# Performance work log

Hardware: AMD Instinct MI355X
Metric: run time of the kernel (lower is better)

The kernel has to match this reference:

```python
import jax, jax.numpy as jnp
import numpy as np

B, T, C, H = 2, 2048, 1024, 16
HD = C // H  # 64
EPS = 1e-5


def _ln(x, g, b):
    mu = jnp.mean(x, axis=-1, keepdims=True)
    var = jnp.var(x, axis=-1, keepdims=True)
    return (x - mu) * jax.lax.rsqrt(var + EPS) * g + b


def setup_inputs() -> dict:
    key = jax.random.key(0)
    ks = jax.random.split(key, 8)
    s = lambda n: 1.0 / np.sqrt(n)
    return {
        "x": jax.random.normal(ks[0], (B, T, C), dtype=jnp.float32),
        "ln1_g": jnp.ones((C,), jnp.float32), "ln1_b": jnp.zeros((C,), jnp.float32),
        "ln2_g": jnp.ones((C,), jnp.float32), "ln2_b": jnp.zeros((C,), jnp.float32),
        "w_in": jax.random.normal(ks[1], (C, 3 * C), jnp.float32) * s(C),
        "b_in": jnp.zeros((3 * C,), jnp.float32),
        "w_out": jax.random.normal(ks[2], (C, C), jnp.float32) * s(C),
        "b_out": jnp.zeros((C,), jnp.float32),
        "w_fc": jax.random.normal(ks[3], (C, 4 * C), jnp.float32) * s(C),
        "b_fc": jnp.zeros((4 * C,), jnp.float32),
        "w_proj": jax.random.normal(ks[4], (4 * C, C), jnp.float32) * s(4 * C),
        "b_proj": jnp.zeros((C,), jnp.float32),
    }


def reference(x, ln1_g, ln1_b, ln2_g, ln2_b, w_in, b_in, w_out, b_out,
              w_fc, b_fc, w_proj, b_proj):
    # --- residual 1: x + attn(ln1(x)) ---
    h = _ln(x, ln1_g, ln1_b)
    qkv = h @ w_in + b_in                          # (B,T,3C)
    # reshape to (B,T,H,3*HD) then chunk per head (matches torch code exactly)
    qkv = qkv.reshape(B, T, H, 3 * HD).transpose(0, 2, 1, 3)  # (B,H,T,3*HD)
    q, k, v = jnp.split(qkv, 3, axis=-1)           # each (B,H,T,HD)
    att = jnp.einsum('bhqd,bhkd->bhqk', q, k) / np.sqrt(HD)
    causal = jnp.tril(jnp.ones((T, T), bool))
    att = jnp.where(causal, att, -jnp.inf)
    att = jax.nn.softmax(att, axis=-1)
    o = jnp.einsum('bhqk,bhkd->bhqd', att, v)      # (B,H,T,HD)
    o = o.transpose(0, 2, 1, 3).reshape(B, T, C)
    x1 = x + (o @ w_out + b_out)
    # --- ln2 applied to residual stream, then residual 2 on top of ln2 output ---
    y = _ln(x1, ln2_g, ln2_b)
    mlp = jax.nn.gelu(y @ w_fc + b_fc, approximate=False) @ w_proj + b_proj
    return y + mlp
```

## Files before the change

### kernel.cpp

```cpp
#include <hip/hip_runtime.h>
#include <hip/hip_bf16.h>
#include <math.h>

typedef __bf16 bf16;
typedef __bf16 bf16x8 __attribute__((ext_vector_type(8)));
typedef __bf16 bf16x4 __attribute__((ext_vector_type(4)));
typedef float floatx4 __attribute__((ext_vector_type(4)));

#define B_ 2
#define T_ 2048
#define C_ 1024
#define H_ 16
#define HD_ 64


__device__ __forceinline__ void gload_lds16(const bf16* g, bf16* l) {
    __builtin_amdgcn_global_load_lds(
        (const __attribute__((address_space(1))) unsigned int*)(g),
        (__attribute__((address_space(3))) unsigned int*)(l), 16, 0, 0);
}

__global__ __launch_bounds__(256) void transpose_all(
        const float* __restrict__ w_in, const float* __restrict__ w_out,
        const float* __restrict__ w_fc, const float* __restrict__ w_proj,
        bf16* __restrict__ o_in, bf16* __restrict__ o_out,
        bf16* __restrict__ o_fc, bf16* __restrict__ o_proj) {
    __shared__ float shf[64 * 33];
    int t = blockIdx.x;
    int tid = threadIdx.x;
    if (t < 7168) {
        const float* src; bf16* dst; int K, N, idx;
        if (t < 3072) { src = w_in; dst = o_in; K = 1024; N = 3072; idx = t; }
        else          { src = w_fc; dst = o_fc; K = 1024; N = 4096; idx = t - 3072; }
        int ntx = N >> 5;
        int nt = (idx % ntx) * 32, kt = (idx / ntx) * 32;
        int tx = tid & 31, ty = tid >> 5;
        #pragma unroll
        for (int i = 0; i < 32; i += 8)
            shf[(ty + i) * 33 + tx] = src[(size_t)(kt + ty + i) * N + nt + tx];
        __syncthreads();
        #pragma unroll
        for (int i = 0; i < 32; i += 8)
            dst[(size_t)(nt + ty + i) * K + kt + tx] = (bf16)shf[tx * 33 + ty + i];
    } else {
        const float* src; bf16* dst; int K, idx;
        if (t < 7680) { src = w_out;  dst = o_out;  K = 1024; idx = t - 7168; }
        else          { src = w_proj; dst = o_proj; K = 4096; idx = t - 7680; }
        const int N = 1024;
        int n0 = (idx & 31) * 32, k0 = (idx >> 5) * 64;
        int col = tid & 31, kr = tid >> 5;
        #pragma unroll
        for (int s = 0; s < 8; s++)
            shf[(kr + s * 8) * 33 + col] = src[(size_t)(k0 + kr + s * 8) * N + n0 + col];
        __syncthreads();
        int tl = tid >> 6, l = tid & 63;
        int ntl = tl & 1, kcl = tl >> 1;
        int rr = ntl * 16 + (l & 15);
        int qd = l >> 4;
        bf16x8 v;
        #pragma unroll
        for (int e = 0; e < 8; e++)
            v[e] = (bf16)shf[(kcl * 32 + qd * 8 + e) * 33 + rr];
        size_t nt_g = (n0 >> 4) + ntl, kc_g = (k0 >> 5) + kcl;
        *(bf16x8*)(dst + (nt_g * (K >> 5) + kc_g) * 512 + l * 8) = v;
    }
}

__global__ __launch_bounds__(256) void ln_kernel(const float* __restrict__ x,
                                                 const float* __restrict__ g,
                                                 const float* __restrict__ b,
                                                 bf16* __restrict__ out_b,
                                                 float* __restrict__ out_f) {
    int row = blockIdx.x;
    int tid = threadIdx.x;
    const float* xr = x + (size_t)row * C_;
    float4 v = ((const float4*)xr)[tid];
    float s  = v.x + v.y + v.z + v.w;
    float ss = v.x * v.x + v.y * v.y + v.z * v.z + v.w * v.w;
    #pragma unroll
    for (int off = 32; off; off >>= 1) {
        s  += __shfl_down(s, off);
        ss += __shfl_down(ss, off);
    }
    __shared__ float red[8];
    int wid = tid >> 6;
    if ((tid & 63) == 0) { red[wid] = s; red[wid + 4] = ss; }
    __syncthreads();
    s  = red[0] + red[1] + red[2] + red[3];
    ss = red[4] + red[5] + red[6] + red[7];
    float mean = s * (1.0f / C_);
    float var  = ss * (1.0f / C_) - mean * mean;
    float rstd = rsqrtf(var + 1e-5f);
    float4 gv = ((const float4*)g)[tid];
    float4 bv = ((const float4*)b)[tid];
    float o0 = (v.x - mean) * rstd * gv.x + bv.x;
    float o1 = (v.y - mean) * rstd * gv.y + bv.y;
    float o2 = (v.z - mean) * rstd * gv.z + bv.z;
    float o3 = (v.w - mean) * rstd * gv.w + bv.w;
    bf16x4 ob = { (bf16)o0, (bf16)o1, (bf16)o2, (bf16)o3 };
    ((bf16x4*)out_b)[(size_t)row * 256 + tid] = ob;
    if (out_f) {
        float4 of; of.x = o0; of.y = o1; of.z = o2; of.w = o3;
        ((float4*)out_f)[(size_t)row * 256 + tid] = of;
    }
}

__device__ __forceinline__ float gelu_fast(float x) {
    float z2 = 1.5957691216f * (x + 0.044715f * x * x * x);
    float e = __expf(z2);
    float t = 1.0f - 2.0f * __builtin_amdgcn_rcpf(e + 1.0f);
    return 0.5f * x * (1.0f + t);
}

template<int MODE>
__global__ __launch_bounds__(256) void gemm128(const bf16* __restrict__ A,
                                               const bf16* __restrict__ Bt,
                                               const float* __restrict__ bias,
                                               void* __restrict__ out,
                                               int M, int N, int K) {
    __shared__ __align__(16) bf16 smem[2 * 128 * 64];
    bf16* As = smem;
    bf16* Bs = smem + 128 * 64;

    int m0 = blockIdx.y * 128, n0 = blockIdx.x * 128;
    int tid = threadIdx.x;
    int wid = __builtin_amdgcn_readfirstlane(tid >> 6);
    int lane = tid & 63;
    int lm = lane & 15, quad = lane >> 4;
    int wm = (wid & 1) * 64;
    int wn = (wid >> 1) * 64;
    int lrow = lane >> 3;
    int lcol = (((lane & 7) ^ lrow)) * 8;

    const bf16* Ablk = A  + (size_t)m0 * K;
    const bf16* Bblk = Bt + (size_t)n0 * K;

    floatx4 acc[4][4];
    #pragma unroll
    for (int i = 0; i < 4; i++)
        #pragma unroll
        for (int j = 0; j < 4; j++) { floatx4 z = {0.f, 0.f, 0.f, 0.f}; acc[i][j] = z; }

    for (int k0 = 0; k0 < K; k0 += 64) {
        __syncthreads();
        #pragma unroll
        for (int c = 0; c < 4; c++) {
            int row = wid * 32 + c * 8;
            gload_lds16(Ablk + (size_t)(row + lrow) * K + k0 + lcol, As + row * 64);
        }
        #pragma unroll
        for (int c = 0; c < 4; c++) {
            int row = wid * 32 + c * 8;
            gload_lds16(Bblk + (size_t)(row + lrow) * K + k0 + lcol, Bs + row * 64);
        }
        __syncthreads();
        #pragma unroll
        for (int kc = 0; kc < 2; kc++) {
            bf16x8 af[4], bfr[4];
            #pragma unroll
            for (int i = 0; i < 4; i++)
                af[i] = *(const bf16x8*)(As + (wm + i * 16 + lm) * 64 +
                                         ((((kc << 2) + quad) ^ (lm & 7)) << 3));
            #pragma unroll
            for (int j = 0; j < 4; j++)
                bfr[j] = *(const bf16x8*)(Bs + (wn + j * 16 + lm) * 64 +
                                          ((((kc << 2) + quad) ^ (lm & 7)) << 3));
            #pragma unroll
            for (int i = 0; i < 4; i++)
                #pragma unroll
                for (int j = 0; j < 4; j++)
                    acc[i][j] = __builtin_amdgcn_mfma_f32_16x16x32_bf16(af[i], bfr[j], acc[i][j], 0, 0, 0);
        }
    }

    if (MODE == 0) {
        #pragma unroll
        for (int i = 0; i < 4; i++)
            #pragma unroll
            for (int j = 0; j < 4; j++) {
                int mbase = m0 + wm + i * 16 + quad * 4;
                int n     = n0 + wn + j * 16 + lm;
                float bsn = bias[n];
                #pragma unroll
                for (int r = 0; r < 4; r++)
                    ((bf16*)out)[(size_t)(mbase + r) * N + n] = (bf16)(acc[i][j][r] + bsn);
            }
    } else {
        bf16* ob = (bf16*)out;
        #pragma unroll
        for (int nh = 0; nh < 2; nh++) {
            __syncthreads();
            if ((wn >> 6) == nh) {
                #pragma unroll
                for (int i = 0; i < 4; i++)
                    #pragma unroll
                    for (int j = 0; j < 4; j++) {
                        int n = n0 + wn + j * 16 + lm;
                        float bsn = bias[n];
                        #pragma unroll
                        for (int r = 0; r < 4; r++)
                            smem[(wm + i * 16 + quad * 4 + r) * 68 + j * 16 + lm] =
                                (bf16)gelu_fast(acc[i][j][r] + bsn);
                    }
            }
            __syncthreads();
            #pragma unroll
            for (int p = 0; p < 4; p++) {
                int tl = wid * 4 + p;
                int mtl = tl >> 1, kclp = tl & 1;
                bf16x8 v = *(const bf16x8*)&smem[(mtl * 16 + lm) * 68 + kclp * 32 + quad * 8];
                int kcl = nh * 2 + kclp;
                *(bf16x8*)(ob + (((size_t)((m0 >> 4) + mtl) * (N >> 5) + (n0 >> 5) + kcl) * 512)
                           + lane * 8) = v;
            }
        }
    }
}

__global__ __launch_bounds__(256) void gemm_direct(const bf16* __restrict__ Af,
                                                   const bf16* __restrict__ Bf,
                                                   const float* __restrict__ bias,
                                                   const float* __restrict__ add,
                                                   float* __restrict__ out,
                                                   int M, int N, int K) {
    int lin = blockIdx.x;
    int xcd = lin & 7, loc = lin >> 3;
    int m0 = ((xcd << 2) | (loc & 3)) * 128;
    int n0 = (loc >> 2) * 64;
    int tid = threadIdx.x;
    int wid = __builtin_amdgcn_readfirstlane(tid >> 6);
    int lane = tid & 63;
    int lm = lane & 15, quad = lane >> 4;
    int wm = (wid & 1) * 64, wn = (wid >> 1) * 32;
    int KC = K >> 5;
    const bf16* Ab = Af + ((size_t)((m0 + wm) >> 4) * KC) * 512 + lane * 8;
    const bf16* Bb = Bf + ((size_t)((n0 + wn) >> 4) * KC) * 512 + lane * 8;

    floatx4 acc[4][2];
    #pragma unroll
    for (int i = 0; i < 4; i++)
        #pragma unroll
        for (int j = 0; j < 2; j++) { floatx4 z = {0.f, 0.f, 0.f, 0.f}; acc[i][j] = z; }

    bf16x8 ac[4][2], bc[2][2], an[4][2], bn[2][2];
    #pragma unroll
    for (int i = 0; i < 4; i++)
        #pragma unroll
        for (int c = 0; c < 2; c++)
            ac[i][c] = *(const bf16x8*)(Ab + ((size_t)i * KC + c) * 512);
    #pragma unroll
    for (int j = 0; j < 2; j++)
        #pragma unroll
        for (int c = 0; c < 2; c++)
            bc[j][c] = *(const bf16x8*)(Bb + ((size_t)j * KC + c) * 512);

    for (int kc0 = 0; kc0 < KC; kc0 += 2) {
        bool pre = (kc0 + 2) < KC;
        if (pre) {
            #pragma unroll
            for (int i = 0; i < 4; i++)
                #pragma unroll
                for (int c = 0; c < 2; c++)
                    an[i][c] = *(const bf16x8*)(Ab + ((size_t)i * KC + kc0 + 2 + c) * 512);
            #pragma unroll
            for (int j = 0; j < 2; j++)
                #pragma unroll
                for (int c = 0; c < 2; c++)
                    bn[j][c] = *(const bf16x8*)(Bb + ((size_t)j * KC + kc0 + 2 + c) * 512);
        }
        #pragma unroll
        for (int c = 0; c < 2; c++)
            #pragma unroll
            for (int i = 0; i < 4; i++)
                #pragma unroll
                for (int j = 0; j < 2; j++)
                    acc[i][j] = __builtin_amdgcn_mfma_f32_16x16x32_bf16(ac[i][c], bc[j][c], acc[i][j], 0, 0, 0);
        if (pre) {
            #pragma unroll
            for (int i = 0; i < 4; i++)
                #pragma unroll
                for (int c = 0; c < 2; c++) ac[i][c] = an[i][c];
            #pragma unroll
            for (int j = 0; j < 2; j++)
                #pragma unroll
                for (int c = 0; c < 2; c++) bc[j][c] = bn[j][c];
        }
    }

    #pragma unroll
    for (int i = 0; i < 4; i++)
        #pragma unroll
        for (int j = 0; j < 2; j++) {
            int mbase = m0 + wm + i * 16 + quad * 4;
            int n     = n0 + wn + j * 16 + lm;
            float bsn = bias[n];
            #pragma unroll
            for (int r = 0; r < 4; r++) {
                size_t idx = (size_t)(mbase + r) * N + n;
                out[idx] = acc[i][j][r] + bsn + add[idx];
            }
        }
}

#define QT_ 128
#define KT_ 64

__global__ __launch_bounds__(512) void attn_mfma_kernel(const bf16* __restrict__ qkv,
                                                        bf16* __restrict__ of) {
    int bh = blockIdx.x;
    int b = bh >> 4, h = bh & 15;
    int q0 = (gridDim.y - 1 - blockIdx.y) * QT_;
    int tid = threadIdx.x, wid = tid >> 6, lane = tid & 63;
    int lm = lane & 15, quad = lane >> 4;
    int sw = lm & 7;
    int r0 = q0 + wid * 16;

    const bf16* base = qkv + (size_t)b * T_ * (3 * C_) + h * (3 * HD_);

    __shared__ __align__(16) bf16 Ks[KT_][72];
    __shared__ __align__(16) bf16 Vt[HD_][72];
    __shared__ __align__(16) bf16 PsT[8][16][64];

    bf16x8 qf[2];
    #pragma unroll
    for (int kc = 0; kc < 2; kc++) {
        bf16x8 t = *(const bf16x8*)(base + (size_t)(r0 + lm) * (3 * C_) + kc * 32 + quad * 8);
        #pragma unroll
        for (int e = 0; e < 8; e++) t[e] = (bf16)((float)t[e] * 0.125f);
        qf[kc] = t;
    }

    floatx4 acc_o[4];
    #pragma unroll
    for (int dn = 0; dn < 4; dn++) { floatx4 z = {0.f, 0.f, 0.f, 0.f}; acc_o[dn] = z; }
    float mst = -1e30f, lst = 0.0f;

    int srow = tid >> 3;
    int scol = (tid & 7) * 8;

    int kmax = q0 + QT_;
    for (int k0 = 0; k0 < kmax; k0 += KT_) {
        bf16x8 kv = *(const bf16x8*)(base + (size_t)(k0 + srow) * (3 * C_) + HD_ + scol);
        bf16x8 vv = *(const bf16x8*)(base + (size_t)(k0 + srow) * (3 * C_) + 2 * HD_ + scol);
        __syncthreads();
        *(bf16x8*)(&Ks[srow][scol]) = kv;
        {
            int c = scol >> 3;
            int pk = ((srow >> 3) ^ c) * 8 + (srow & 7);
            #pragma unroll
            for (int j = 0; j < 8; j++) Vt[scol + j][pk] = vv[j];
        }
        __syncthreads();

        if (k0 <= r0 + 15) {
            floatx4 st[4];
            #pragma unroll
            for (int bn = 0; bn < 4; bn++) { floatx4 z = {0.f, 0.f, 0.f, 0.f}; st[bn] = z; }
            #pragma unroll
            for (int kc = 0; kc < 2; kc++) {
                bf16x8 kf[4];
                #pragma unroll
                for (int bn = 0; bn < 4; bn++)
                    kf[bn] = *(const bf16x8*)(&Ks[bn * 16 + lm][kc * 32 + quad * 8]);
                #pragma unroll
                for (int bn = 0; bn < 4; bn++)
                    st[bn] = __builtin_amdgcn_mfma_f32_16x16x32_bf16(kf[bn], qf[kc], st[bn], 0, 0, 0);
            }

            float vv_[4][4];
            float rm = -1e30f;
            if (k0 + KT_ - 1 > r0) {
                int gq = r0 + lm;
                #pragma unroll
                for (int bn = 0; bn < 4; bn++)
                    #pragma unroll
                    for (int r = 0; r < 4; r++) {
                        int key = k0 + bn * 16 + quad * 4 + r;
                        float sv = (key <= gq) ? st[bn][r] : -1e30f;
                        vv_[bn][r] = sv;
                        rm = fmaxf(rm, sv);
                    }
            } else {
                #pragma unroll
                for (int bn = 0; bn < 4; bn++)
                    #pragma unroll
                    for (int r = 0; r < 4; r++) {
                        vv_[bn][r] = st[bn][r];
                        rm = fmaxf(rm, st[bn][r]);
                    }
            }
            rm = fmaxf(rm, __shfl_xor(rm, 16));
            rm = fmaxf(rm, __shfl_xor(rm, 32));
            float mnew = fmaxf(mst, rm);
            float alpha = __expf(mst - mnew);
            mst = mnew;
            float ps = 0.f;
            #pragma unroll
            for (int bn = 0; bn < 4; bn++) {
                float p0 = __expf(vv_[bn][0] - mnew);
                float p1 = __expf(vv_[bn][1] - mnew);
                float p2 = __expf(vv_[bn][2] - mnew);
                float p3 = __expf(vv_[bn][3] - mnew);
                ps += (p0 + p1) + (p2 + p3);
                bf16x4 pk = { (bf16)p0, (bf16)p1, (bf16)p2, (bf16)p3 };
                int kb = bn * 2 + (quad >> 1);
                int col = ((kb ^ sw) << 3) + (quad & 1) * 4;
                *(bf16x4*)(&PsT[wid][lm][col]) = pk;
            }
            ps += __shfl_xor(ps, 16);
            ps += __shfl_xor(ps, 32);
            lst = lst * alpha + ps;

            #pragma unroll
            for (int r = 0; r < 4; r++) {
                float ar = __shfl(alpha, quad * 4 + r);
                #pragma unroll
                for (int dn = 0; dn < 4; dn++) acc_o[dn][r] *= ar;
            }

            __asm__ volatile("s_waitcnt lgkmcnt(0)" ::: "memory");

            #pragma unroll
            for (int kc = 0; kc < 2; kc++) {
                bf16x8 pa = *(const bf16x8*)(&PsT[wid][lm][((kc * 4 + quad) ^ sw) << 3]);
                bf16x8 vfr[4];
                #pragma unroll
                for (int dn = 0; dn < 4; dn++) {
                    int d = dn * 16 + lm;
                    int swd = (d >> 3) & 7;
                    vfr[dn] = *(const bf16x8*)(&Vt[d][(((kc * 4 + quad) ^ swd) << 3)]);
                }
                #pragma unroll
                for (int dn = 0; dn < 4; dn++)
                    acc_o[dn] = __builtin_amdgcn_mfma_f32_16x16x32_bf16(pa, vfr[dn], acc_o[dn], 0, 0, 0);
            }
        }
    }

    float il = 1.0f / lst;
    #pragma unroll
    for (int r = 0; r < 4; r++) {
        float ir = __shfl(il, quad * 4 + r);
        #pragma unroll
        for (int dn = 0; dn < 4; dn++)
            PsT[wid][quad * 4 + r][dn * 16 + lm] = (bf16)(acc_o[dn][r] * ir);
    }
    __asm__ volatile("s_waitcnt lgkmcnt(0)" ::: "memory");
    size_t mtb = ((size_t)b * T_ + r0) >> 4;
    #pragma unroll
    for (int kcl = 0; kcl < 2; kcl++) {
        bf16x8 v = *(const bf16x8*)&PsT[wid][lm][kcl * 32 + quad * 8];
        *(bf16x8*)(of + (mtb * (C_ >> 5) + (h * 2 + kcl)) * 512 + lane * 8) = v;
    }
}

extern "C" void kernel_launch(void* const* d_in, const int* in_sizes, int n_in,
                              void* d_out, int out_size, void* d_ws, size_t ws_size,
                              hipStream_t stream) {
    (void)in_sizes; (void)n_in; (void)out_size; (void)ws_size;
    const float* x      = (const float*)d_in[0];
    const float* ln1_g  = (const float*)d_in[1];
    const float* ln1_b  = (const float*)d_in[2];
    const float* ln2_g  = (const float*)d_in[3];
    const float* ln2_b  = (const float*)d_in[4];
    const float* w_in   = (const float*)d_in[5];
    const float* b_in   = (const float*)d_in[6];
    const float* w_out  = (const float*)d_in[7];
    const float* b_out  = (const float*)d_in[8];
    const float* w_fc   = (const float*)d_in[9];
    const float* b_fc   = (const float*)d_in[10];
    const float* w_proj = (const float*)d_in[11];
    const float* b_proj = (const float*)d_in[12];

    char* ws = (char*)d_ws;
    const size_t MB = 1024 * 1024;
    bf16*  w_inT   = (bf16*)(ws + 0);
    bf16*  w_outF  = (bf16*)(ws + 6 * MB);
    bf16*  w_fcT   = (bf16*)(ws + 8 * MB);
    bf16*  w_projF = (bf16*)(ws + 16 * MB);
    bf16*  qkv     = (bf16*)(ws + 24 * MB);
    bf16*  fc_frag = (bf16*)(ws + 24 * MB);
    bf16*  o_frag  = (bf16*)(ws + 56 * MB);
    bf16*  y_b     = (bf16*)(ws + 56 * MB);
    bf16*  h_b     = (bf16*)(ws + 64 * MB);
    float* x1      = (float*)(ws + 64 * MB);
    float* y_f     = (float*)(ws + 80 * MB);

    const int M = B_ * T_;

    transpose_all<<<9728, 256, 0, stream>>>(w_in, w_out, w_fc, w_proj,
                                            w_inT, w_outF, w_fcT, w_projF);

    ln_kernel<<<M, 256, 0, stream>>>(x, ln1_g, ln1_b, h_b, nullptr);
    gemm128<0><<<dim3(3 * C_ / 128, M / 128), 256, 0, stream>>>(h_b, w_inT, b_in,
                                                                qkv, M, 3 * C_, C_);
    attn_mfma_kernel<<<dim3(B_ * H_, T_ / QT_), 512, 0, stream>>>(qkv, o_frag);
    gemm_direct<<<512, 256, 0, stream>>>(o_frag, w_outF, b_out, x, x1, M, C_, C_);
    ln_kernel<<<M, 256, 0, stream>>>(x1, ln2_g, ln2_b, y_b, y_f);
    gemm128<1><<<dim3(4 * C_ / 128, M / 128), 256, 0, stream>>>(y_b, w_fcT, b_fc,
                                                                fc_frag, M, 4 * C_, C_);
    gemm_direct<<<512, 256, 0, stream>>>(fc_frag, w_projF, b_proj, y_f,
                                         (float*)d_out, M, C_, 4 * C_);
}
```

Before: 350.9 us.

## Replace 128-tile GEMM with double-buffered 256x256 pipelined GEMM and triple-buffer direct GEMM

The QKV and FC GEMMs move from a 128x128, single-buffered LDS kernel to a 256x256-tile, 512-thread kernel. It double-buffers A/B in LDS, interleaves async global-to-LDS loads with quarter-tile MFMA groups, uses explicit barriers and vmcnt waits, raises wave priority around the MFMAs, and remaps blocks across XCDs. The direct-fragment GEMM gets a three-stage register prefetch ring in place of two stages. The aim is to hide memory latency and raise MFMA utilisation. The cost is much higher register and LDS use (128 KB smem) and fewer, larger blocks, which could hurt occupancy or tail balance.

```diff
diff --git a/kernel.cpp b/kernel.cpp
--- a/kernel.cpp
+++ b/kernel.cpp
@@ -112,117 +112,186 @@
     return 0.5f * x * (1.0f + t);
 }
 
+#define BAR() do { __builtin_amdgcn_sched_barrier(0); __builtin_amdgcn_s_barrier(); __builtin_amdgcn_sched_barrier(0); } while (0)
+#define VMC6() asm volatile("s_waitcnt vmcnt(6)" ::: "memory")
+#define VMC0() asm volatile("s_waitcnt vmcnt(0)" ::: "memory")
+
+#define LOAD_A(AS, QM) \
+  { _Pragma("unroll") for (int i_ = 0; i_ < 4; i_++) { \
+      const int r_ = wm128 + ((QM) * 4 + i_) * 16 + lm; \
+      _Pragma("unroll") for (int kc_ = 0; kc_ < 2; kc_++) \
+        aR[i_][kc_] = *(const bf16x8*)((AS) + r_ * 64 + ((((kc_ << 2) | quad) ^ (lm & 7)) << 3)); } }
+
+#define LOAD_B(BS, QN) \
+  { _Pragma("unroll") for (int j_ = 0; j_ < 2; j_++) { \
+      const int r_ = wn64 + ((QN) * 2 + j_) * 16 + lm; \
+      _Pragma("unroll") for (int kc_ = 0; kc_ < 2; kc_++) \
+        bR[QN][j_][kc_] = *(const bf16x8*)((BS) + r_ * 64 + ((((kc_ << 2) | quad) ^ (lm & 7)) << 3)); } }
+
+#define MFMA_Q(QM, QN) \
+  { __builtin_amdgcn_s_setprio(1); \
+    _Pragma("unroll") for (int i_ = 0; i_ < 4; i_++) \
+    _Pragma("unroll") for (int j_ = 0; j_ < 2; j_++) \
+    _Pragma("unroll") for (int kc_ = 0; kc_ < 2; kc_++) \
+      acc[(QM) * 4 + i_][(QN) * 2 + j_] = __builtin_amdgcn_mfma_f32_16x16x32_bf16( \
+          aR[i_][kc_], bR[QN][j_][kc_], acc[(QM) * 4 + i_][(QN) * 2 + j_], 0, 0, 0); \
+    __builtin_amdgcn_s_setprio(0); }
+
+#define STG(gb, lb, r0v, k0v) \
+    gload_lds16((gb) + (size_t)((r0v) + sr8) * K + (k0v) + scb, (lb) + ((r0v) + wid * 8) * 64)
+
 template<int MODE>
-__global__ __launch_bounds__(256) void gemm128(const bf16* __restrict__ A,
-                                               const bf16* __restrict__ Bt,
-                                               const float* __restrict__ bias,
-                                               void* __restrict__ out,
-                                               int M, int N, int K) {
-    __shared__ __align__(16) bf16 smem[2 * 128 * 64];
-    bf16* As = smem;
-    bf16* Bs = smem + 128 * 64;
-
-    int m0 = blockIdx.y * 128, n0 = blockIdx.x * 128;
+__global__ __launch_bounds__(512, 2) void gemm256(const bf16* __restrict__ A,
+                                                  const bf16* __restrict__ Bt,
+                                                  const float* __restrict__ bias,
+                                                  void* __restrict__ out,
+                                                  int M, int N, int K) {
+    (void)M;
+    __shared__ __align__(16) bf16 smem[4 * 256 * 64];
+    bf16* As0 = smem;
+    bf16* Bs0 = smem + 1 * 256 * 64;
+    bf16* As1 = smem + 2 * 256 * 64;
+    bf16* Bs1 = smem + 3 * 256 * 64;
+
+    int ntn = N >> 8;
+    int lin = blockIdx.x;
+    int id  = (lin & 7) * (gridDim.x >> 3) + (lin >> 3);
+    int mt = id / ntn, nt = id - mt * ntn;
+    int m0 = mt << 8, n0 = nt << 8;
+
     int tid = threadIdx.x;
     int wid = __builtin_amdgcn_readfirstlane(tid >> 6);
     int lane = tid & 63;
     int lm = lane & 15, quad = lane >> 4;
-    int wm = (wid & 1) * 64;
-    int wn = (wid >> 1) * 64;
-    int lrow = lane >> 3;
-    int lcol = (((lane & 7) ^ lrow)) * 8;
+    int wm128 = (wid & 1) * 128;
+    int wn64  = (wid >> 1) * 64;
 
     const bf16* Ablk = A  + (size_t)m0 * K;
     const bf16* Bblk = Bt + (size_t)n0 * K;
 
-    floatx4 acc[4][4];
-    #pragma unroll
-    for (int i = 0; i < 4; i++)
-        #pragma unroll
-        for (int j = 0; j < 4; j++) { floatx4 z = {0.f, 0.f, 0.f, 0.f}; acc[i][j] = z; }
-
-    for (int k0 = 0; k0 < K; k0 += 64) {
-        __syncthreads();
-        #pragma unroll
-        for (int c = 0; c < 4; c++) {
-            int row = wid * 32 + c * 8;
-            gload_lds16(Ablk + (size_t)(row + lrow) * K + k0 + lcol, As + row * 64);
-        }
-        #pragma unroll
-        for (int c = 0; c < 4; c++) {
-            int row = wid * 32 + c * 8;
-            gload_lds16(Bblk + (size_t)(row + lrow) * K + k0 + lcol, Bs + row * 64);
-        }
-        __syncthreads();
-        #pragma unroll
-        for (int kc = 0; kc < 2; kc++) {
-            bf16x8 af[4], bfr[4];
-            #pragma unroll
-            for (int i = 0; i < 4; i++)
-                af[i] = *(const bf16x8*)(As + (wm + i * 16 + lm) * 64 +
-                                         ((((kc << 2) + quad) ^ (lm & 7)) << 3));
-            #pragma unroll
-            for (int j = 0; j < 4; j++)
-                bfr[j] = *(const bf16x8*)(Bs + (wn + j * 16 + lm) * 64 +
-                                          ((((kc << 2) + quad) ^ (lm & 7)) << 3));
-            #pragma unroll
-            for (int i = 0; i < 4; i++)
-                #pragma unroll
-                for (int j = 0; j < 4; j++)
-                    acc[i][j] = __builtin_amdgcn_mfma_f32_16x16x32_bf16(af[i], bfr[j], acc[i][j], 0, 0, 0);
-        }
+    int sr8 = wid * 8 + (lane >> 3);
+    int scb = ((lane & 7) ^ (lane >> 3)) << 3;
+
+    floatx4 acc[8][4];
+    #pragma unroll
+    for (int f = 0; f < 8; f++)
+        #pragma unroll
+        for (int g = 0; g < 4; g++) { floatx4 z = {0.f, 0.f, 0.f, 0.f}; acc[f][g] = z; }
+    bf16x8 aR[4][2], bR[2][2][2];
+
+    int nI = K >> 7;
+
+    STG(Ablk, As0, 0, 0);   STG(Ablk, As0, 64, 0);
+    STG(Ablk, As0, 128, 0); STG(Ablk, As0, 192, 0);
+    STG(Bblk, Bs0, 0, 0);   STG(Bblk, Bs0, 64, 0);
+    STG(Bblk, Bs0, 128, 0); STG(Bblk, Bs0, 192, 0);
+    STG(Ablk, As1, 0, 64);  STG(Ablk, As1, 128, 64);
+    STG(Bblk, Bs1, 0, 64);  STG(Bblk, Bs1, 64, 64);
+    STG(Ablk, As1, 64, 64); STG(Ablk, As1, 192, 64);
+    VMC6();
+    BAR();
+
+    for (int it = 0; it < nI; it++) {
+        int kE = (2 * it + 2) << 6;
+        int kO = (2 * it + 3) << 6;
+        int kT = (2 * it + 1) << 6;
+        bool nl = (it + 1 < nI);
+        LOAD_A(As0, 0); LOAD_B(Bs0, 0);
+        STG(Bblk, Bs1, 128, kT); STG(Bblk, Bs1, 192, kT);
+        BAR(); MFMA_Q(0, 0); BAR();
+        LOAD_B(Bs0, 1);
+        if (nl) { STG(Ablk, As0, 0, kE); STG(Ablk, As0, 128, kE); }
+        BAR(); MFMA_Q(0, 1); BAR();
+        LOAD_A(As0, 1);
+        if (nl) { STG(Bblk, Bs0, 0, kE); STG(Bblk, Bs0, 64, kE); }
+        BAR(); MFMA_Q(1, 0); BAR();
+        if (nl) { STG(Ablk, As0, 64, kE); STG(Ablk, As0, 192, kE); }
+        BAR(); MFMA_Q(1, 1);
+        if (nl) { VMC6(); } else { VMC0(); }
+        BAR();
+        LOAD_A(As1, 0); LOAD_B(Bs1, 0);
+        if (nl) { STG(Bblk, Bs0, 128, kE); STG(Bblk, Bs0, 192, kE); }
+        BAR(); MFMA_Q(0, 0); BAR();
+        LOAD_B(Bs1, 1);
+        if (nl) { STG(Ablk, As1, 0, kO); STG(Ablk, As1, 128, kO); }
+        BAR(); MFMA_Q(0, 1); BAR();
+        LOAD_A(As1, 1);
+        if (nl) { STG(Bblk, Bs1, 0, kO); STG(Bblk, Bs1, 64, kO); }
+        BAR(); MFMA_Q(1, 0); BAR();
+        if (nl) { STG(Ablk, As1, 64, kO); STG(Ablk, As1, 192, kO); }
+        BAR(); MFMA_Q(1, 1);
+        if (nl) { VMC6(); }
+        BAR();
     }
 
     if (MODE == 0) {
-        #pragma unroll
-        for (int i = 0; i < 4; i++)
-            #pragma unroll
-            for (int j = 0; j < 4; j++) {
-                int mbase = m0 + wm + i * 16 + quad * 4;
-                int n     = n0 + wn + j * 16 + lm;
+        bf16* ob = (bf16*)out;
+        #pragma unroll
+        for (int f = 0; f < 8; f++) {
+            int row0 = m0 + wm128 + f * 16 + quad * 4;
+            #pragma unroll
+            for (int g = 0; g < 4; g++) {
+                int n = n0 + wn64 + g * 16 + lm;
                 float bsn = bias[n];
                 #pragma unroll
                 for (int r = 0; r < 4; r++)
-                    ((bf16*)out)[(size_t)(mbase + r) * N + n] = (bf16)(acc[i][j][r] + bsn);
-            }
+                    ob[(size_t)(row0 + r) * N + n] = (bf16)(acc[f][g][r] + bsn);
+            }
+        }
     } else {
         bf16* ob = (bf16*)out;
-        #pragma unroll
-        for (int nh = 0; nh < 2; nh++) {
-            __syncthreads();
-            if ((wn >> 6) == nh) {
-                #pragma unroll
-                for (int i = 0; i < 4; i++)
+        bf16* patch = smem + wid * (64 * 68);
+        size_t mtb = (size_t)((m0 + wm128) >> 4);
+        int ncb = (n0 + wn64) >> 5;
+        #pragma unroll
+        for (int h = 0; h < 2; h++) {
+            #pragma unroll
+            for (int ff = 0; ff < 4; ff++)
+                #pragma unroll
+                for (int g = 0; g < 4; g++) {
+                    int n = n0 + wn64 + g * 16 + lm;
+                    float bsn = bias[n];
                     #pragma unroll
-                    for (int j = 0; j < 4; j++) {
-                        int n = n0 + wn + j * 16 + lm;
-                        float bsn = bias[n];
-                        #pragma unroll
-                        for (int r = 0; r < 4; r++)
-                            smem[(wm + i * 16 + quad * 4 + r) * 68 + j * 16 + lm] =
-                                (bf16)gelu_fast(acc[i][j][r] + bsn);
-                    }
-            }
-            __syncthreads();
-            #pragma unroll
-            for (int p = 0; p < 4; p++) {
-                int tl = wid * 4 + p;
-                int mtl = tl >> 1, kclp = tl & 1;
-                bf16x8 v = *(const bf16x8*)&smem[(mtl * 16 + lm) * 68 + kclp * 32 + quad * 8];
-                int kcl = nh * 2 + kclp;
-                *(bf16x8*)(ob + (((size_t)((m0 >> 4) + mtl) * (N >> 5) + (n0 >> 5) + kcl) * 512)
-                           + lane * 8) = v;
-            }
-        }
-    }
-}
-
-__global__ __launch_bounds__(256) void gemm_direct(const bf16* __restrict__ Af,
-                                                   const bf16* __restrict__ Bf,
-                                                   const float* __restrict__ bias,
-                                                   const float* __restrict__ add,
-                                                   float* __restrict__ out,
-                                                   int M, int N, int K) {
+                    for (int r = 0; r < 4; r++)
+                        patch[(ff * 16 + quad * 4 + r) * 68 + g * 16 + lm] =
+                            (bf16)gelu_fast(acc[h * 4 + ff][g][r] + bsn);
+                }
+            #pragma unroll
+            for (int ff = 0; ff < 4; ff++)
+                #pragma unroll
+                for (int kc = 0; kc < 2; kc++) {
+                    bf16x8 v = *(const bf16x8*)&patch[(ff * 16 + lm) * 68 + kc * 32 + quad * 8];
+                    size_t tile = (mtb + h * 4 + ff) * (size_t)(N >> 5) + ncb + kc;
+                    *(bf16x8*)(ob + tile * 512 + lane * 8) = v;
+                }
+        }
+    }
+}
+
+#define GD_STEP(BUF, SS) \
+  if ((SS) < S) { \
+    int kp_ = 2 * (SS) + 4; \
+    if (kp_ < KC) { \
+      _Pragma("unroll") for (int i_ = 0; i_ < 4; i_++) \
+        _Pragma("unroll") for (int c_ = 0; c_ < 2; c_++) \
+          ab[((BUF) + 2) % 3][i_][c_] = *(const bf16x8*)(Ab + ((size_t)i_ * KC + kp_ + c_) * 512); \
+      _Pragma("unroll") for (int j_ = 0; j_ < 2; j_++) \
+        _Pragma("unroll") for (int c_ = 0; c_ < 2; c_++) \
+          bb[((BUF) + 2) % 3][j_][c_] = *(const bf16x8*)(Bb + ((size_t)j_ * KC + kp_ + c_) * 512); \
+    } \
+    _Pragma("unroll") for (int c_ = 0; c_ < 2; c_++) \
+      _Pragma("unroll") for (int i_ = 0; i_ < 4; i_++) \
+        _Pragma("unroll") for (int j_ = 0; j_ < 2; j_++) \
+          acc[i_][j_] = __builtin_amdgcn_mfma_f32_16x16x32_bf16(ab[BUF][i_][c_], bb[BUF][j_][c_], acc[i_][j_], 0, 0, 0); \
+  }
+
+__global__ __launch_bounds__(256, 2) void gemm_direct(const bf16* __restrict__ Af,
+                                                      const bf16* __restrict__ Bf,
+                                                      const float* __restrict__ bias,
+                                                      const float* __restrict__ add,
+                                                      float* __restrict__ out,
+                                                      int M, int N, int K) {
+    (void)M;
     int lin = blockIdx.x;
     int xcd = lin & 7, loc = lin >> 3;
     int m0 = ((xcd << 2) | (loc & 3)) * 128;
@@ -242,49 +311,26 @@
         #pragma unroll
         for (int j = 0; j < 2; j++) { floatx4 z = {0.f, 0.f, 0.f, 0.f}; acc[i][j] = z; }
 
-    bf16x8 ac[4][2], bc[2][2], an[4][2], bn[2][2];
-    #pragma unroll
-    for (int i = 0; i < 4; i++)
-        #pragma unroll
-        for (int c = 0; c < 2; c++)
-            ac[i][c] = *(const bf16x8*)(Ab + ((size_t)i * KC + c) * 512);
-    #pragma unroll
-    for (int j = 0; j < 2; j++)
-        #pragma unroll
-        for (int c = 0; c < 2; c++)
-            bc[j][c] = *(const bf16x8*)(Bb + ((size_t)j * KC + c) * 512);
-
-    for (int kc0 = 0; kc0 < KC; kc0 += 2) {
-        bool pre = (kc0 + 2) < KC;
-        if (pre) {
-            #pragma unroll
-            for (int i = 0; i < 4; i++)
-                #pragma unroll
-                for (int c = 0; c < 2; c++)
-                    an[i][c] = *(const bf16x8*)(Ab + ((size_t)i * KC + kc0 + 2 + c) * 512);
-            #pragma unroll
-            for (int j = 0; j < 2; j++)
-                #pragma unroll
-                for (int c = 0; c < 2; c++)
-                    bn[j][c] = *(const bf16x8*)(Bb + ((size_t)j * KC + kc0 + 2 + c) * 512);
-        }
-        #pragma unroll
-        for (int c = 0; c < 2; c++)
-            #pragma unroll
-            for (int i = 0; i < 4; i++)
-                #pragma unroll
-                for (int j = 0; j < 2; j++)
-                    acc[i][j] = __builtin_amdgcn_mfma_f32_16x16x32_bf16(ac[i][c], bc[j][c], acc[i][j], 0, 0, 0);
-        if (pre) {
-            #pragma unroll
-            for (int i = 0; i < 4; i++)
-                #pragma unroll
-                for (int c = 0; c < 2; c++) ac[i][c] = an[i][c];
-            #pragma unroll
-            for (int j = 0; j < 2; j++)
-                #pragma unroll
-                for (int c = 0; c < 2; c++) bc[j][c] = bn[j][c];
-        }
+    bf16x8 ab[3][4][2], bb[3][2][2];
+    #pragma unroll
+    for (int c = 0; c < 2; c++) {
+        #pragma unroll
+        for (int i = 0; i < 4; i++) {
+            ab[0][i][c] = *(const bf16x8*)(Ab + ((size_t)i * KC + c) * 512);
+            ab[1][i][c] = *(const bf16x8*)(Ab + ((size_t)i * KC + 2 + c) * 512);
+        }
+        #pragma unroll
+        for (int j = 0; j < 2; j++) {
+            bb[0][j][c] = *(const bf16x8*)(Bb + ((size_t)j * KC + c) * 512);
+            bb[1][j][c] = *(const bf16x8*)(Bb + ((size_t)j * KC + 2 + c) * 512);
+        }
+    }
+
+    int S = KC >> 1;
+    for (int s0 = 0; s0 < S; s0 += 3) {
+        GD_STEP(0, s0);
+        GD_STEP(1, s0 + 1);
+        GD_STEP(2, s0 + 2);
     }
 
     #pragma unroll
@@ -492,13 +538,13 @@
                                             w_inT, w_outF, w_fcT, w_projF);
 
     ln_kernel<<<M, 256, 0, stream>>>(x, ln1_g, ln1_b, h_b, nullptr);
-    gemm128<0><<<dim3(3 * C_ / 128, M / 128), 256, 0, stream>>>(h_b, w_inT, b_in,
-                                                                qkv, M, 3 * C_, C_);
+    gemm256<0><<<(M >> 8) * ((3 * C_) >> 8), 512, 0, stream>>>(h_b, w_inT, b_in,
+                                                               qkv, M, 3 * C_, C_);
     attn_mfma_kernel<<<dim3(B_ * H_, T_ / QT_), 512, 0, stream>>>(qkv, o_frag);
     gemm_direct<<<512, 256, 0, stream>>>(o_frag, w_outF, b_out, x, x1, M, C_, C_);
     ln_kernel<<<M, 256, 0, stream>>>(x1, ln2_g, ln2_b, y_b, y_f);
-    gemm128<1><<<dim3(4 * C_ / 128, M / 128), 256, 0, stream>>>(y_b, w_fcT, b_fc,
-                                                                fc_frag, M, 4 * C_, C_);
+    gemm256<1><<<(M >> 8) * ((4 * C_) >> 8), 512, 0, stream>>>(y_b, w_fcT, b_fc,
+                                                               fc_frag, M, 4 * C_, C_);
     gemm_direct<<<512, 256, 0, stream>>>(fc_frag, w_projF, b_proj, y_f,
                                          (float*)d_out, M, C_, 4 * C_);
 }
```

After: 330.0 us. -6.0%, faster.
